# Performance work log

Measured on AMD Instinct MI355X. Metric: run time of the kernel, lower is better.

## Reference

```python
import jax, jax.numpy as jnp
import numpy as np

NEG = -1e30  # log-space 'zero' (avoid real -inf for stable exp/grad)


def _ctc_loss_mean(logp, targets, target_lengths, blank):
    """CTC loss, PyTorch semantics (reduction='mean', zero_infinity=True).
    logp: (B, T, V) log-probabilities; targets: (B, L) padded labels;
    target_lengths: (B,) ints. All input lengths are T (uniform here).
    """
    B, T, V = logp.shape
    L = targets.shape[1]
    S = 2 * L + 1  # extended label length: blank-interleaved

    ext = jnp.full((B, S), blank, dtype=targets.dtype)
    ext = ext.at[:, 1::2].set(targets)  # blanks at even s, labels at odd s

    s = jnp.arange(S)
    valid = s[None, :] < (2 * target_lengths + 1)[:, None]  # (B, S)
    prev2 = jnp.pad(ext[:, :-2], ((0, 0), (2, 0)), constant_values=blank)
    # skip transition s-2 -> s allowed only at non-blank s with no label repeat
    allow_skip = (s[None, :] >= 2) & (ext != blank) & (ext != prev2)

    # per-(t, s) emission log-prob, masked outside valid extended labels
    emit = jnp.take_along_axis(
        logp, jnp.broadcast_to(ext[:, None, :], (B, T, S)), axis=2
    )  # (B, T, S)
    emit = jnp.where(valid[:, None, :], emit, NEG)

    alpha0 = jnp.full((B, S), NEG, dtype=logp.dtype)
    alpha0 = alpha0.at[:, 0].set(emit[:, 0, 0])
    alpha0 = alpha0.at[:, 1].set(emit[:, 0, 1])

    def step(alpha, e):
        a1 = alpha
        a2 = jnp.pad(alpha[:, :-1], ((0, 0), (1, 0)), constant_values=NEG)
        a3 = jnp.pad(alpha[:, :-2], ((0, 0), (2, 0)), constant_values=NEG)
        a3 = jnp.where(allow_skip, a3, NEG)
        m = jnp.maximum(jnp.maximum(a1, a2), a3)
        new = m + jnp.log(jnp.exp(a1 - m) + jnp.exp(a2 - m) + jnp.exp(a3 - m)) + e
        return new, None

    alpha, _ = jax.lax.scan(step, alpha0, jnp.swapaxes(emit, 0, 1)[1:])

    i1 = (2 * target_lengths).astype(jnp.int32)
    l1 = jnp.take_along_axis(alpha, i1[:, None], axis=1)[:, 0]
    l2 = jnp.take_along_axis(alpha, jnp.maximum(i1 - 1, 0)[:, None], axis=1)[:, 0]
    l2 = jnp.where(target_lengths > 0, l2, NEG)
    m = jnp.maximum(l1, l2)
    loss = -(m + jnp.log(jnp.exp(l1 - m) + jnp.exp(l2 - m)))  # (B,)
    loss = jnp.where(loss > 1e20, 0.0, loss)  # zero_infinity=True
    # reduction='mean': divide by target length, then batch mean
    return jnp.mean(loss / jnp.maximum(target_lengths, 1).astype(loss.dtype))


def setup_inputs() -> dict:
    key = jax.random.key(0)
    kl, kt, kn = jax.random.split(key, 3)
    B, T, V, L = 32, 1024, 1000, 256
    logits = jax.random.normal(kl, (B, T, V), dtype=jnp.float32)
    targets = jax.random.randint(kt, (B, L), 1, V).astype(jnp.int32)
    lengths = jax.random.randint(kn, (B,), L // 2 + 2, L + 1)
    target_padding_mask = jnp.arange(L)[None, :] < lengths[:, None]  # bool (B, L)
    return {"logits": logits, "targets": targets,
            "target_padding_mask": target_padding_mask}


def reference(logits, targets, target_padding_mask):
    blank = 0
    lg = logits[:, :-1, :]            # drop last frame
    tgt = targets[:, 1:]              # drop leading (SOS) token
    logp = jax.nn.log_softmax(lg, axis=-1)  # (B, T-1, V)
    tlen = target_padding_mask.sum(axis=1).astype(jnp.int32) - 1
    return _ctc_loss_mean(logp, tgt, tlen, blank)
```

## Files before the change

kernel.cpp:

```cpp
#include <hip/hip_runtime.h>

#define LOG2E 1.4426950408889634f
#define LN2   0.6931471805599453

static constexpr int B  = 32;
static constexpr int T  = 1024;
static constexpr int TT = 1023;
static constexpr int V  = 1000;
static constexpr int L  = 256;
static constexpr int S  = 511;
static constexpr int LP = 256;
static constexpr int TP = 1024;

using hf2 = __attribute__((ext_vector_type(2))) __fp16;
using f4  = __attribute__((ext_vector_type(4))) float;
using i4  = __attribute__((ext_vector_type(4))) int;
using i2  = __attribute__((ext_vector_type(2))) int;

__device__ __forceinline__ float fexp2(float x) {
#if __has_builtin(__builtin_amdgcn_exp2f)
  return __builtin_amdgcn_exp2f(x);
#else
  return exp2f(x);
#endif
}
__device__ __forceinline__ float flog2(float x) {
#if __has_builtin(__builtin_amdgcn_logf)
  return __builtin_amdgcn_logf(x);
#else
  return log2f(x);
#endif
}

#if __has_builtin(__builtin_amdgcn_update_dpp)
__device__ __forceinline__ float shr1f(float x) {
  int r = __builtin_amdgcn_update_dpp(0, __float_as_int(x), 0x138, 0xf, 0xf, true);
  return __int_as_float(r);
}
__device__ __forceinline__ int shl1i(int x) {
  return __builtin_amdgcn_update_dpp(0, x, 0x130, 0xf, 0xf, true);
}
#define DPP_SWITCH(T, OLD, SRC, BC)                                            \
  T r;                                                                         \
  switch (ctrl) {                                                              \
    case 0x111: r = __builtin_amdgcn_update_dpp(OLD, SRC, 0x111, 0xf, 0xf, BC); break; \
    case 0x112: r = __builtin_amdgcn_update_dpp(OLD, SRC, 0x112, 0xf, 0xf, BC); break; \
    case 0x114: r = __builtin_amdgcn_update_dpp(OLD, SRC, 0x114, 0xf, 0xf, BC); break; \
    case 0x118: r = __builtin_amdgcn_update_dpp(OLD, SRC, 0x118, 0xf, 0xf, BC); break; \
    case 0x142: r = __builtin_amdgcn_update_dpp(OLD, SRC, 0x142, 0xf, 0xf, BC); break; \
    default:    r = __builtin_amdgcn_update_dpp(OLD, SRC, 0x143, 0xf, 0xf, BC); break; \
  }

__device__ __forceinline__ int dppmax_step(int m, const int ctrl) {
  DPP_SWITCH(int, 0, m, true);
  return max(m, r);
}
__device__ __forceinline__ int wavemax_to_sgpr(int m) {
  m = dppmax_step(m, 0x111);
  m = dppmax_step(m, 0x112);
  m = dppmax_step(m, 0x114);
  m = dppmax_step(m, 0x118);
  m = dppmax_step(m, 0x142);
  m = dppmax_step(m, 0x143);
  return __builtin_amdgcn_readlane(m, 63);
}
__device__ __forceinline__ float dppfmax_step(float x, const int ctrl) {
  int xi = __float_as_int(x);
  DPP_SWITCH(int, xi, xi, false);
  return fmaxf(x, __int_as_float(r));
}
__device__ __forceinline__ float wavefmax(float x) {
  x = dppfmax_step(x, 0x111);
  x = dppfmax_step(x, 0x112);
  x = dppfmax_step(x, 0x114);
  x = dppfmax_step(x, 0x118);
  x = dppfmax_step(x, 0x142);
  x = dppfmax_step(x, 0x143);
  return __int_as_float(__builtin_amdgcn_readlane(__float_as_int(x), 63));
}
__device__ __forceinline__ float dppfadd_step(float x, const int ctrl) {
  DPP_SWITCH(int, 0, __float_as_int(x), true);
  return x + __int_as_float(r);
}
__device__ __forceinline__ float wavefsum(float x) {
  x = dppfadd_step(x, 0x111);
  x = dppfadd_step(x, 0x112);
  x = dppfadd_step(x, 0x114);
  x = dppfadd_step(x, 0x118);
  x = dppfadd_step(x, 0x142);
  x = dppfadd_step(x, 0x143);
  return __int_as_float(__builtin_amdgcn_readlane(__float_as_int(x), 63));
}
#else
__device__ __forceinline__ float shr1f(float x) {
  float r = __shfl_up(x, 1, 64);
  return (threadIdx.x & 63) == 0 ? 0.0f : r;
}
__device__ __forceinline__ int shl1i(int x) {
  int r = __shfl_down(x, 1, 64);
  return (threadIdx.x & 63) == 63 ? 0 : r;
}
__device__ __forceinline__ int wavemax_to_sgpr(int m) {
  for (int o = 32; o >= 1; o >>= 1) m = max(m, __shfl_xor(m, o, 64));
  return m;
}
__device__ __forceinline__ float wavefmax(float x) {
  for (int o = 32; o >= 1; o >>= 1) x = fmaxf(x, __shfl_xor(x, o, 64));
  return x;
}
__device__ __forceinline__ float wavefsum(float x) {
  for (int o = 32; o >= 1; o >>= 1) x += __shfl_xor(x, o, 64);
  return x;
}
#endif

__device__ __forceinline__ int mask_tlen(const unsigned char* maskb, int b, int lane) {
  int ca = 0;
  for (int k = lane; k < L; k += 64) ca += (maskb[b * L + k] != 0) ? 1 : 0;
  for (int o = 32; o >= 1; o >>= 1) ca += __shfl_xor(ca, o, 64);
  int cnt = ca;
  if (ca < 130) {
    const int* mi = (const int*)maskb;
    int cb = 0;
    for (int k = lane; k < L; k += 64) cb += (mi[b * L + k] != 0) ? 1 : 0;
    for (int o = 32; o >= 1; o >>= 1) cb += __shfl_xor(cb, o, 64);
    cnt = cb;
  }
  return cnt - 1;
}

__global__ __launch_bounds__(256) void k_emit(const float* __restrict__ logits,
                                              const int* __restrict__ targets,
                                              _Float16* __restrict__ EL,
                                              _Float16* __restrict__ EBs,
                                              float* __restrict__ I2,
                                              float* __restrict__ G) {
  __shared__ float yrow[4][1024];
  const int wid = threadIdx.x >> 6;
  const int lane = threadIdx.x & 63;
  float* yw = yrow[wid];
  const int r = blockIdx.x * 4 + wid;
  const int b = r / TT;
  const int t = r - b * TT;

  const f4* row = reinterpret_cast<const f4*>(logits + ((size_t)b * T + t) * V);
  f4 u0 = row[lane];
  f4 u1 = row[lane + 64];
  f4 u2 = row[lane + 128];
  const bool has3 = (lane < 58);
  f4 u3;
  if (has3) u3 = row[lane + 192];
  else { u3[0] = u3[1] = u3[2] = u3[3] = -3.0e38f; }

  reinterpret_cast<f4*>(yw)[lane]       = u0;
  reinterpret_cast<f4*>(yw)[lane + 64]  = u1;
  reinterpret_cast<f4*>(yw)[lane + 128] = u2;
  if (has3) reinterpret_cast<f4*>(yw)[lane + 192] = u3;

  float lm = fmaxf(fmaxf(fmaxf(u0[0], u0[1]), fmaxf(u0[2], u0[3])),
                   fmaxf(fmaxf(u1[0], u1[1]), fmaxf(u1[2], u1[3])));
  lm = fmaxf(lm, fmaxf(fmaxf(u2[0], u2[1]), fmaxf(u2[2], u2[3])));
  lm = fmaxf(lm, fmaxf(fmaxf(u3[0], u3[1]), fmaxf(u3[2], u3[3])));
  const float my = wavefmax(lm);
  const float c = -my * LOG2E;

  float ps = fexp2(fmaf(u0[0], LOG2E, c)) + fexp2(fmaf(u0[1], LOG2E, c))
           + fexp2(fmaf(u0[2], LOG2E, c)) + fexp2(fmaf(u0[3], LOG2E, c))
           + fexp2(fmaf(u1[0], LOG2E, c)) + fexp2(fmaf(u1[1], LOG2E, c))
           + fexp2(fmaf(u1[2], LOG2E, c)) + fexp2(fmaf(u1[3], LOG2E, c))
           + fexp2(fmaf(u2[0], LOG2E, c)) + fexp2(fmaf(u2[1], LOG2E, c))
           + fexp2(fmaf(u2[2], LOG2E, c)) + fexp2(fmaf(u2[3], LOG2E, c))
           + fexp2(fmaf(u3[0], LOG2E, c)) + fexp2(fmaf(u3[1], LOG2E, c))
           + fexp2(fmaf(u3[2], LOG2E, c)) + fexp2(fmaf(u3[3], LOG2E, c));
  const float g = -flog2(wavefsum(ps));

  const int base = b * L + (lane << 2);
  i4 tv = *reinterpret_cast<const i4*>(targets + base);
  const int l1 = tv[1], l2 = tv[2], l3 = tv[3];
  const int l4 = shl1i(tv[0]);
  const float eb = fexp2(fmaf(yw[0],  LOG2E, c));
  const float e1 = fexp2(fmaf(yw[l1], LOG2E, c));
  const float e2 = fexp2(fmaf(yw[l2], LOG2E, c));
  const float e3 = fexp2(fmaf(yw[l3], LOG2E, c));
  float e4       = fexp2(fmaf(yw[l4], LOG2E, c));
  if (lane == 63) e4 = 0.0f;

  i2 oi;
#if __has_builtin(__builtin_amdgcn_cvt_pkrtz)
  { hf2 p = __builtin_amdgcn_cvt_pkrtz(e1, e2); oi[0] = __builtin_bit_cast(int, p); }
  { hf2 p = __builtin_amdgcn_cvt_pkrtz(e3, e4); oi[1] = __builtin_bit_cast(int, p); }
#else
  { hf2 p; p[0] = (__fp16)e1; p[1] = (__fp16)e2; oi[0] = __builtin_bit_cast(int, p); }
  { hf2 p; p[0] = (__fp16)e3; p[1] = (__fp16)e4; oi[1] = __builtin_bit_cast(int, p); }
#endif
  reinterpret_cast<i2*>(EL + ((size_t)b * TP + t) * LP)[lane] = oi;
  if (lane == 0) {
    G[r] = g;
    if (t > 0) EBs[b * TP + (t - 1)] = (_Float16)eb;
    else { I2[2 * b] = eb; I2[2 * b + 1] = e1; }
  }
}

__global__ __launch_bounds__(64, 1) void k_ctc(const _Float16* __restrict__ EL,
                                               const _Float16* __restrict__ EBs,
                                               const int* __restrict__ targets,
                                               const unsigned char* __restrict__ maskb,
                                               const float* __restrict__ G,
                                               const float* __restrict__ I2,
                                               float* __restrict__ lossb) {
  const int b = blockIdx.x;
  const int lane = threadIdx.x;
  const int s0 = lane << 3;
  const int* tg = targets + b * L;

  const int tl = mask_tlen(maskb, b, lane);

  float f1 = 0.0f, f3, f5, f7 = 0.0f;
  {
    int s = s0 + 1;
    if (s >= 3) f1 = (tg[(s + 1) >> 1] != tg[(s - 1) >> 1]) ? 1.0f : 0.0f;
    s = s0 + 3;
    f3 = (tg[(s + 1) >> 1] != tg[(s - 1) >> 1]) ? 1.0f : 0.0f;
    s = s0 + 5;
    f5 = (tg[(s + 1) >> 1] != tg[(s - 1) >> 1]) ? 1.0f : 0.0f;
    s = s0 + 7;
    if (s < S) f7 = (tg[(s + 1) >> 1] != tg[(s - 1) >> 1]) ? 1.0f : 0.0f;
  }

  const int s2t = 2 * tl;
  const int vm0 = (s0 + 0 <= s2t) ? -1 : 0;
  const int vm1 = (s0 + 1 <= s2t) ? -1 : 0;
  const int vm2 = (s0 + 2 <= s2t) ? -1 : 0;
  const int vm3 = (s0 + 3 <= s2t) ? -1 : 0;
  const int vm4 = (s0 + 4 <= s2t) ? -1 : 0;
  const int vm5 = (s0 + 5 <= s2t) ? -1 : 0;
  const int vm6 = (s0 + 6 <= s2t) ? -1 : 0;
  const int vm7 = (s0 + 7 <= s2t) ? -1 : 0;

  const _Float16* ELb = EL + (size_t)b * TP * LP + (lane << 2);
  const _Float16* EBb = EBs + b * TP;

  float a0 = (lane == 0) ? I2[2 * b]     : 0.0f;
  float a1 = (lane == 0) ? I2[2 * b + 1] : 0.0f;
  float a2 = 0.f, a3 = 0.f, a4 = 0.f, a5 = 0.f, a6 = 0.f, a7 = 0.f;
  float n7 = 0.0f;
  int lsacc = 0;

  asm volatile("" :: "v"(f1), "v"(f3), "v"(f5), "v"(f7),
                     "v"(a0), "v"(a1), "v"((float)tl));

#define LOAD8(P, r0)                                             \
  do {                                                           \
    const _Float16* ql_ = ELb + (size_t)(r0) * LP;               \
    const _Float16* qb_ = EBb + ((r0) - 1);                      \
    asm volatile(                                                \
      "global_load_dwordx2 %0, %9, off\n\t"                      \
      "global_load_dwordx2 %1, %9, off offset:512\n\t"           \
      "global_load_dwordx2 %2, %9, off offset:1024\n\t"          \
      "global_load_dwordx2 %3, %9, off offset:1536\n\t"          \
      "global_load_dwordx2 %4, %9, off offset:2048\n\t"          \
      "global_load_dwordx2 %5, %9, off offset:2560\n\t"          \
      "global_load_dwordx2 %6, %9, off offset:3072\n\t"          \
      "global_load_dwordx2 %7, %9, off offset:3584\n\t"          \
      "global_load_dwordx4 %8, %10, off"                         \
      : "=&v"(P##0), "=&v"(P##1), "=&v"(P##2), "=&v"(P##3),      \
        "=&v"(P##4), "=&v"(P##5), "=&v"(P##6), "=&v"(P##7),      \
        "=&v"(P##Q)                                              \
      : "v"(ql_), "v"(qb_));                                     \
  } while (0)

#define VMWAIT8(n, P)                                            \
  do {                                                           \
    asm volatile("s_waitcnt vmcnt(" #n ")"                       \
                 : "+v"(P##0), "+v"(P##1), "+v"(P##2), "+v"(P##3), \
                   "+v"(P##4), "+v"(P##5), "+v"(P##6), "+v"(P##7), \
                   "+v"(P##Q));                                  \
    __builtin_amdgcn_sched_barrier(0);                           \
  } while (0)

#define MIXLO(D, SSS, HWORD)                                     \
  asm("v_fma_mix_f32 %0, %1, %2, 0 op_sel:[0,0,0] op_sel_hi:[0,1,0]" \
      : "=v"(D) : "v"(SSS), "v"(HWORD))
#define MIXHI(D, SSS, HWORD)                                     \
  asm("v_fma_mix_f32 %0, %1, %2, 0 op_sel:[0,1,0] op_sel_hi:[0,1,0]" \
      : "=v"(D) : "v"(SSS), "v"(HWORD))

#define STEP_IMPL(H, BD, BMIX)                                  \
  do {                                                          \
    float s7_ = fmaf(f7, a5, a6 + a7);                          \
    float t7; MIXHI(t7, s7_, (H)[1]);                   \
    float n7n = shr1f(t7);                                      \
    float s0_ = a0 + n7;                                        \
    float s1_ = fmaf(f1, n7, a0 + a1);                          \
    float s2_ = a1 + a2;                                        \
    float s3_ = fmaf(f3, a1, a2 + a3);                          \
    float s4_ = a3 + a4;                                        \
    float s5_ = fmaf(f5, a3, a4 + a5);                          \
    float s6_ = a5 + a6;                                        \
    float t0, t1, t2, t3, t4, t5, t6;                           \
    BMIX(t0, s0_, (BD));                             \
    MIXLO(t1, s1_, (H)[0]);                             \
    BMIX(t2, s2_, (BD));                                        \
    MIXHI(t3, s3_, (H)[0]);                             \
    BMIX(t4, s4_, (BD));                                        \
    MIXLO(t5, s5_, (H)[1]);                             \
    BMIX(t6, s6_, (BD));                                        \
    a0 = t0; a1 = t1; a2 = t2; a3 = t3;                         \
    a4 = t4; a5 = t5; a6 = t6; a7 = t7;                         \
    n7 = n7n;                                                   \
  } while (0)
#define STEPFL(H, BD) STEP_IMPL(H, BD, MIXLO)
#define STEPFH(H, BD) STEP_IMPL(H, BD, MIXHI)

#define RESCALE()                                               \
  do {                                                          \
    int m = max(max(max(__float_as_int(a0) & vm0,               \
                        __float_as_int(a1) & vm1),              \
                    max(__float_as_int(a2) & vm2,               \
                        __float_as_int(a3) & vm3)),             \
                max(max(__float_as_int(a4) & vm4,               \
                        __float_as_int(a5) & vm5),              \
                    max(__float_as_int(a6) & vm6,               \
                        __float_as_int(a7) & vm7)));            \
    int mw = wavemax_to_sgpr(m);                                \
    int e = mw >> 23;                                           \
    int sh = 191 - e;                                           \
    lsacc += e - 191;                                           \
    a0 = ldexpf(a0, sh); a1 = ldexpf(a1, sh);                   \
    a2 = ldexpf(a2, sh); a3 = ldexpf(a3, sh);                   \
    a4 = ldexpf(a4, sh); a5 = ldexpf(a5, sh);                   \
    a6 = ldexpf(a6, sh); a7 = ldexpf(a7, sh);                   \
    n7 = ldexpf(n7, sh);                                        \
  } while (0)

#define PROC8(P)                                                \
  do {                                                          \
    STEPFL(P##0, P##Q[0]); STEPFH(P##1, P##Q[0]);               \
    STEPFL(P##2, P##Q[1]); STEPFH(P##3, P##Q[1]);               \
    STEPFL(P##4, P##Q[2]); STEPFH(P##5, P##Q[2]);               \
    STEPFL(P##6, P##Q[3]); STEPFH(P##7, P##Q[3]);               \
  } while (0)

  i2 A0, A1, A2, A3, A4, A5, A6, A7; i4 AQ;
  i2 B0, B1, B2, B3, B4, B5, B6, B7; i4 BQ;
  i2 C0, C1, C2, C3, C4, C5, C6, C7; i4 CQ;
  i2 D0, D1, D2, D3, D4, D5, D6, D7; i4 DQ;

  LOAD8(A, 1);
  LOAD8(B, 9);
  LOAD8(C, 17);
  LOAD8(D, 25);

  int t = 1;
#pragma unroll 1
  for (int it = 0; it < 30; ++it) {
    RESCALE();
    VMWAIT8(27, A); PROC8(A); LOAD8(A, t + 32);
    VMWAIT8(27, B); PROC8(B); LOAD8(B, t + 40);
    VMWAIT8(27, C); PROC8(C); LOAD8(C, t + 48);
    VMWAIT8(27, D); PROC8(D); LOAD8(D, t + 56);
    t += 32;
  }
  RESCALE();
  VMWAIT8(27, A); PROC8(A); LOAD8(A, 993);
  VMWAIT8(27, B); PROC8(B); LOAD8(B, 1001);
  VMWAIT8(27, C); PROC8(C); LOAD8(C, 1009);
  VMWAIT8(27, D); PROC8(D); LOAD8(D, 1017);
  RESCALE();
  VMWAIT8(27, A); PROC8(A);
  VMWAIT8(18, B); PROC8(B);
  VMWAIT8(9,  C); PROC8(C);
  VMWAIT8(0,  D);
  STEPFL(D0, DQ[0]); STEPFH(D1, DQ[0]);
  STEPFL(D2, DQ[1]); STEPFH(D3, DQ[1]);
  STEPFL(D4, DQ[2]); STEPFH(D5, DQ[2]);
#undef LOAD8
#undef VMWAIT8
#undef MIXLO
#undef MIXHI
#undef STEP_IMPL
#undef STEPFL
#undef STEPFH
#undef RESCALE
#undef PROC8

  double gs = 0.0;
  for (int k = lane; k < TT; k += 64) gs += (double)G[b * TT + k];
  for (int o = 32; o >= 1; o >>= 1) gs += __shfl_xor(gs, o, 64);

  {
    int i1 = 2 * tl;
    int j1 = (i1 > 0 ? i1 : 1) - 1;
    float va, vb;
    switch (i1 & 7) {
      case 0: va = a0; break; case 1: va = a1; break;
      case 2: va = a2; break; case 3: va = a3; break;
      case 4: va = a4; break; case 5: va = a5; break;
      case 6: va = a6; break; default: va = a7; break;
    }
    switch (j1 & 7) {
      case 0: vb = a0; break; case 1: vb = a1; break;
      case 2: vb = a2; break; case 3: vb = a3; break;
      case 4: vb = a4; break; case 5: vb = a5; break;
      case 6: vb = a6; break; default: vb = a7; break;
    }
    float l1v = __shfl(va, i1 >> 3, 64);
    float l2v = __shfl(vb, j1 >> 3, 64);
    if (lane == 0) {
      float p = l1v + l2v;
      int hi = __float_as_int(p);
      int ep = (hi >> 23) - 127;
      float pm = ldexpf(p, -ep);
      float lm = flog2(pm);
      double loss2 = -((double)lm + (double)ep + (double)lsacc + gs);
      float loss = (float)(loss2 * LN2);
      if (!(loss <= 1e20f)) loss = 0.0f;
      int dv = (tl > 0) ? tl : 1;
      lossb[b] = loss / (float)dv;
    }
  }
}

__global__ void k_mean(const float* __restrict__ lossb, float* __restrict__ out) {
  int lane = threadIdx.x;
  float v = (lane < B) ? lossb[lane] : 0.0f;
  for (int o = 32; o >= 1; o >>= 1) v += __shfl_xor(v, o, 64);
  if (lane == 0) out[0] = v / (float)B;
}

extern "C" void kernel_launch(void* const* d_in, const int* in_sizes, int n_in,
                              void* d_out, int out_size, void* d_ws, size_t ws_size,
                              hipStream_t stream) {
  const float* logits = (const float*)d_in[0];
  const int* targets = (const int*)d_in[1];
  const unsigned char* mask = (const unsigned char*)d_in[2];

  char* ws = (char*)d_ws;
  float* lossb = (float*)(ws + 128);
  float* I2 = (float*)(ws + 256);
  float* G = (float*)(ws + 512);
  _Float16* EBs = (_Float16*)(ws + 140 * 1024);
  _Float16* EL = (_Float16*)(ws + 256 * 1024);

  k_emit<<<(B * TT) / 4, 256, 0, stream>>>(logits, targets, EL, EBs, I2, G);
  k_ctc<<<B, 64, 0, stream>>>(EL, EBs, targets, mask, G, I2, lossb);
  k_mean<<<1, 64, 0, stream>>>(lossb, (float*)d_out);
}
```

Baseline: 82.14 us.

## Process two batch items per CTC wavefront with interleaved recurrences

Each k_ctc wavefront now runs the alpha recurrence for two batch elements (b and b+16), interleaving their steps so the two independent dependency chains hide each other's latency. The grid is halved to 16 blocks. The prefetch pipeline is reshaped from four 8-step stages to three per batch item, and the rescale exponent target changes. This trades higher register pressure and half the wavefronts for better instruction-level parallelism in the latency-bound serial scan.

```diff
diff --git a/kernel.cpp b/kernel.cpp
--- a/kernel.cpp
+++ b/kernel.cpp
@@ -208,51 +208,70 @@
                                                const float* __restrict__ G,
                                                const float* __restrict__ I2,
                                                float* __restrict__ lossb) {
-  const int b = blockIdx.x;
+  const int bx = blockIdx.x;
+  const int by = blockIdx.x + 16;
   const int lane = threadIdx.x;
   const int s0 = lane << 3;
-  const int* tg = targets + b * L;
-
-  const int tl = mask_tlen(maskb, b, lane);
-
-  float f1 = 0.0f, f3, f5, f7 = 0.0f;
+  const int* tgx = targets + bx * L;
+  const int* tgy = targets + by * L;
+
+  const int tlx = mask_tlen(maskb, bx, lane);
+  const int tly = mask_tlen(maskb, by, lane);
+
+  float f1x = 0.0f, f3x, f5x, f7x = 0.0f;
+  float f1y = 0.0f, f3y, f5y, f7y = 0.0f;
   {
     int s = s0 + 1;
-    if (s >= 3) f1 = (tg[(s + 1) >> 1] != tg[(s - 1) >> 1]) ? 1.0f : 0.0f;
+    if (s >= 3) {
+      f1x = (tgx[(s + 1) >> 1] != tgx[(s - 1) >> 1]) ? 1.0f : 0.0f;
+      f1y = (tgy[(s + 1) >> 1] != tgy[(s - 1) >> 1]) ? 1.0f : 0.0f;
+    }
     s = s0 + 3;
-    f3 = (tg[(s + 1) >> 1] != tg[(s - 1) >> 1]) ? 1.0f : 0.0f;
+    f3x = (tgx[(s + 1) >> 1] != tgx[(s - 1) >> 1]) ? 1.0f : 0.0f;
+    f3y = (tgy[(s + 1) >> 1] != tgy[(s - 1) >> 1]) ? 1.0f : 0.0f;
     s = s0 + 5;
-    f5 = (tg[(s + 1) >> 1] != tg[(s - 1) >> 1]) ? 1.0f : 0.0f;
+    f5x = (tgx[(s + 1) >> 1] != tgx[(s - 1) >> 1]) ? 1.0f : 0.0f;
+    f5y = (tgy[(s + 1) >> 1] != tgy[(s - 1) >> 1]) ? 1.0f : 0.0f;
     s = s0 + 7;
-    if (s < S) f7 = (tg[(s + 1) >> 1] != tg[(s - 1) >> 1]) ? 1.0f : 0.0f;
-  }
-
-  const int s2t = 2 * tl;
-  const int vm0 = (s0 + 0 <= s2t) ? -1 : 0;
-  const int vm1 = (s0 + 1 <= s2t) ? -1 : 0;
-  const int vm2 = (s0 + 2 <= s2t) ? -1 : 0;
-  const int vm3 = (s0 + 3 <= s2t) ? -1 : 0;
-  const int vm4 = (s0 + 4 <= s2t) ? -1 : 0;
-  const int vm5 = (s0 + 5 <= s2t) ? -1 : 0;
-  const int vm6 = (s0 + 6 <= s2t) ? -1 : 0;
-  const int vm7 = (s0 + 7 <= s2t) ? -1 : 0;
-
-  const _Float16* ELb = EL + (size_t)b * TP * LP + (lane << 2);
-  const _Float16* EBb = EBs + b * TP;
-
-  float a0 = (lane == 0) ? I2[2 * b]     : 0.0f;
-  float a1 = (lane == 0) ? I2[2 * b + 1] : 0.0f;
-  float a2 = 0.f, a3 = 0.f, a4 = 0.f, a5 = 0.f, a6 = 0.f, a7 = 0.f;
-  float n7 = 0.0f;
-  int lsacc = 0;
-
-  asm volatile("" :: "v"(f1), "v"(f3), "v"(f5), "v"(f7),
-                     "v"(a0), "v"(a1), "v"((float)tl));
-
-#define LOAD8(P, r0)                                             \
+    if (s < S) {
+      f7x = (tgx[(s + 1) >> 1] != tgx[(s - 1) >> 1]) ? 1.0f : 0.0f;
+      f7y = (tgy[(s + 1) >> 1] != tgy[(s - 1) >> 1]) ? 1.0f : 0.0f;
+    }
+  }
+
+  const int s2tx = 2 * tlx, s2ty = 2 * tly;
+  const int vm0x = (s0 + 0 <= s2tx) ? -1 : 0, vm0y = (s0 + 0 <= s2ty) ? -1 : 0;
+  const int vm1x = (s0 + 1 <= s2tx) ? -1 : 0, vm1y = (s0 + 1 <= s2ty) ? -1 : 0;
+  const int vm2x = (s0 + 2 <= s2tx) ? -1 : 0, vm2y = (s0 + 2 <= s2ty) ? -1 : 0;
+  const int vm3x = (s0 + 3 <= s2tx) ? -1 : 0, vm3y = (s0 + 3 <= s2ty) ? -1 : 0;
+  const int vm4x = (s0 + 4 <= s2tx) ? -1 : 0, vm4y = (s0 + 4 <= s2ty) ? -1 : 0;
+  const int vm5x = (s0 + 5 <= s2tx) ? -1 : 0, vm5y = (s0 + 5 <= s2ty) ? -1 : 0;
+  const int vm6x = (s0 + 6 <= s2tx) ? -1 : 0, vm6y = (s0 + 6 <= s2ty) ? -1 : 0;
+  const int vm7x = (s0 + 7 <= s2tx) ? -1 : 0, vm7y = (s0 + 7 <= s2ty) ? -1 : 0;
+
+  const _Float16* ELbx = EL + (size_t)bx * TP * LP + (lane << 2);
+  const _Float16* ELby = EL + (size_t)by * TP * LP + (lane << 2);
+  const _Float16* EBbx = EBs + bx * TP;
+  const _Float16* EBby = EBs + by * TP;
+
+  float a0x = (lane == 0) ? I2[2 * bx]     : 0.0f;
+  float a1x = (lane == 0) ? I2[2 * bx + 1] : 0.0f;
+  float a2x = 0.f, a3x = 0.f, a4x = 0.f, a5x = 0.f, a6x = 0.f, a7x = 0.f;
+  float a0y = (lane == 0) ? I2[2 * by]     : 0.0f;
+  float a1y = (lane == 0) ? I2[2 * by + 1] : 0.0f;
+  float a2y = 0.f, a3y = 0.f, a4y = 0.f, a5y = 0.f, a6y = 0.f, a7y = 0.f;
+  float n7x = 0.0f, n7y = 0.0f;
+  int lsaccx = 0, lsaccy = 0;
+
+  asm volatile("" :: "v"(f1x), "v"(f3x), "v"(f5x), "v"(f7x),
+                     "v"(f1y), "v"(f3y), "v"(f5y), "v"(f7y),
+                     "v"(a0x), "v"(a1x), "v"(a0y), "v"(a1y),
+                     "v"((float)tlx), "v"((float)tly));
+
+#define LOAD8(P, r0, ELB, EBB)                                   \
   do {                                                           \
-    const _Float16* ql_ = ELb + (size_t)(r0) * LP;               \
-    const _Float16* qb_ = EBb + ((r0) - 1);                      \
+    const _Float16* ql_ = (ELB) + (size_t)(r0) * LP;             \
+    const _Float16* qb_ = (EBB) + ((r0) - 1);                    \
     asm volatile(                                                \
       "global_load_dwordx2 %0, %9, off\n\t"                      \
       "global_load_dwordx2 %1, %9, off offset:512\n\t"           \
@@ -269,12 +288,16 @@
       : "v"(ql_), "v"(qb_));                                     \
   } while (0)
 
-#define VMWAIT8(n, P)                                            \
+#define VMWAIT2(n, PX, PY)                                       \
   do {                                                           \
     asm volatile("s_waitcnt vmcnt(" #n ")"                       \
-                 : "+v"(P##0), "+v"(P##1), "+v"(P##2), "+v"(P##3), \
-                   "+v"(P##4), "+v"(P##5), "+v"(P##6), "+v"(P##7), \
-                   "+v"(P##Q));                                  \
+                 : "+v"(PX##0), "+v"(PX##1), "+v"(PX##2), "+v"(PX##3), \
+                   "+v"(PX##4), "+v"(PX##5), "+v"(PX##6), "+v"(PX##7), \
+                   "+v"(PX##Q));                                 \
+    asm volatile(""                                              \
+                 : "+v"(PY##0), "+v"(PY##1), "+v"(PY##2), "+v"(PY##3), \
+                   "+v"(PY##4), "+v"(PY##5), "+v"(PY##6), "+v"(PY##7), \
+                   "+v"(PY##Q));                                 \
     __builtin_amdgcn_sched_barrier(0);                           \
   } while (0)
 
@@ -285,140 +308,160 @@
   asm("v_fma_mix_f32 %0, %1, %2, 0 op_sel:[0,1,0] op_sel_hi:[0,1,0]" \
       : "=v"(D) : "v"(SSS), "v"(HWORD))
 
-#define STEP_IMPL(H, BD, BMIX)                                  \
+#define STEP_IMPL(H, BD, BMIX, X)                               \
   do {                                                          \
-    float s7_ = fmaf(f7, a5, a6 + a7);                          \
-    float t7; MIXHI(t7, s7_, (H)[1]);                   \
-    float n7n = shr1f(t7);                                      \
-    float s0_ = a0 + n7;                                        \
-    float s1_ = fmaf(f1, n7, a0 + a1);                          \
-    float s2_ = a1 + a2;                                        \
-    float s3_ = fmaf(f3, a1, a2 + a3);                          \
-    float s4_ = a3 + a4;                                        \
-    float s5_ = fmaf(f5, a3, a4 + a5);                          \
-    float s6_ = a5 + a6;                                        \
-    float t0, t1, t2, t3, t4, t5, t6;                           \
-    BMIX(t0, s0_, (BD));                             \
-    MIXLO(t1, s1_, (H)[0]);                             \
-    BMIX(t2, s2_, (BD));                                        \
-    MIXHI(t3, s3_, (H)[0]);                             \
-    BMIX(t4, s4_, (BD));                                        \
-    MIXLO(t5, s5_, (H)[1]);                             \
-    BMIX(t6, s6_, (BD));                                        \
-    a0 = t0; a1 = t1; a2 = t2; a3 = t3;                         \
-    a4 = t4; a5 = t5; a6 = t6; a7 = t7;                         \
-    n7 = n7n;                                                   \
-  } while (0)
-#define STEPFL(H, BD) STEP_IMPL(H, BD, MIXLO)
-#define STEPFH(H, BD) STEP_IMPL(H, BD, MIXHI)
-
-#define RESCALE()                                               \
+    float s7_ = fmaf(f7##X, a5##X, a6##X + a7##X);              \
+    float t7_; MIXHI(t7_, s7_, (H)[1]);                 \
+    float n7n_ = shr1f(t7_);                                    \
+    float s0_ = a0##X + n7##X;                                  \
+    float s1_ = fmaf(f1##X, n7##X, a0##X + a1##X);              \
+    float s2_ = a1##X + a2##X;                                  \
+    float s3_ = fmaf(f3##X, a1##X, a2##X + a3##X);              \
+    float s4_ = a3##X + a4##X;                                  \
+    float s5_ = fmaf(f5##X, a3##X, a4##X + a5##X);              \
+    float s6_ = a5##X + a6##X;                                  \
+    float t0_, t1_, t2_, t3_, t4_, t5_, t6_;                    \
+    BMIX(t0_, s0_, (BD));                            \
+    MIXLO(t1_, s1_, (H)[0]);                            \
+    BMIX(t2_, s2_, (BD));                                       \
+    MIXHI(t3_, s3_, (H)[0]);                            \
+    BMIX(t4_, s4_, (BD));                                       \
+    MIXLO(t5_, s5_, (H)[1]);                            \
+    BMIX(t6_, s6_, (BD));                                       \
+    a0##X = t0_; a1##X = t1_; a2##X = t2_; a3##X = t3_;         \
+    a4##X = t4_; a5##X = t5_; a6##X = t6_; a7##X = t7_;         \
+    n7##X = n7n_;                                               \
+  } while (0)
+#define STEPFL(H, BD, X) STEP_IMPL(H, BD, MIXLO, X)
+#define STEPFH(H, BD, X) STEP_IMPL(H, BD, MIXHI, X)
+
+#define PROC8XY(PX, PY)                                         \
   do {                                                          \
-    int m = max(max(max(__float_as_int(a0) & vm0,               \
-                        __float_as_int(a1) & vm1),              \
-                    max(__float_as_int(a2) & vm2,               \
-                        __float_as_int(a3) & vm3)),             \
-                max(max(__float_as_int(a4) & vm4,               \
-                        __float_as_int(a5) & vm5),              \
-                    max(__float_as_int(a6) & vm6,               \
-                        __float_as_int(a7) & vm7)));            \
+    STEPFL(PX##0, PX##Q[0], x); STEPFL(PY##0, PY##Q[0], y);     \
+    STEPFH(PX##1, PX##Q[0], x); STEPFH(PY##1, PY##Q[0], y);     \
+    STEPFL(PX##2, PX##Q[1], x); STEPFL(PY##2, PY##Q[1], y);     \
+    STEPFH(PX##3, PX##Q[1], x); STEPFH(PY##3, PY##Q[1], y);     \
+    STEPFL(PX##4, PX##Q[2], x); STEPFL(PY##4, PY##Q[2], y);     \
+    STEPFH(PX##5, PX##Q[2], x); STEPFH(PY##5, PY##Q[2], y);     \
+    STEPFL(PX##6, PX##Q[3], x); STEPFL(PY##6, PY##Q[3], y);     \
+    STEPFH(PX##7, PX##Q[3], x); STEPFH(PY##7, PY##Q[3], y);     \
+  } while (0)
+
+#define RESCALE(X)                                              \
+  do {                                                          \
+    int m = max(max(max(__float_as_int(a0##X) & vm0##X,         \
+                        __float_as_int(a1##X) & vm1##X),        \
+                    max(__float_as_int(a2##X) & vm2##X,         \
+                        __float_as_int(a3##X) & vm3##X)),       \
+                max(max(__float_as_int(a4##X) & vm4##X,         \
+                        __float_as_int(a5##X) & vm5##X),        \
+                    max(__float_as_int(a6##X) & vm6##X,         \
+                        __float_as_int(a7##X) & vm7##X)));      \
     int mw = wavemax_to_sgpr(m);                                \
     int e = mw >> 23;                                           \
-    int sh = 191 - e;                                           \
-    lsacc += e - 191;                                           \
-    a0 = ldexpf(a0, sh); a1 = ldexpf(a1, sh);                   \
-    a2 = ldexpf(a2, sh); a3 = ldexpf(a3, sh);                   \
-    a4 = ldexpf(a4, sh); a5 = ldexpf(a5, sh);                   \
-    a6 = ldexpf(a6, sh); a7 = ldexpf(a7, sh);                   \
-    n7 = ldexpf(n7, sh);                                        \
-  } while (0)
-
-#define PROC8(P)                                                \
-  do {                                                          \
-    STEPFL(P##0, P##Q[0]); STEPFH(P##1, P##Q[0]);               \
-    STEPFL(P##2, P##Q[1]); STEPFH(P##3, P##Q[1]);               \
-    STEPFL(P##4, P##Q[2]); STEPFH(P##5, P##Q[2]);               \
-    STEPFL(P##6, P##Q[3]); STEPFH(P##7, P##Q[3]);               \
-  } while (0)
-
-  i2 A0, A1, A2, A3, A4, A5, A6, A7; i4 AQ;
-  i2 B0, B1, B2, B3, B4, B5, B6, B7; i4 BQ;
-  i2 C0, C1, C2, C3, C4, C5, C6, C7; i4 CQ;
-  i2 D0, D1, D2, D3, D4, D5, D6, D7; i4 DQ;
-
-  LOAD8(A, 1);
-  LOAD8(B, 9);
-  LOAD8(C, 17);
-  LOAD8(D, 25);
+    int sh = 203 - e;                                           \
+    lsacc##X += e - 203;                                        \
+    a0##X = ldexpf(a0##X, sh); a1##X = ldexpf(a1##X, sh);       \
+    a2##X = ldexpf(a2##X, sh); a3##X = ldexpf(a3##X, sh);       \
+    a4##X = ldexpf(a4##X, sh); a5##X = ldexpf(a5##X, sh);       \
+    a6##X = ldexpf(a6##X, sh); a7##X = ldexpf(a7##X, sh);       \
+    n7##X = ldexpf(n7##X, sh);                                  \
+  } while (0)
+
+  i2 Ax0, Ax1, Ax2, Ax3, Ax4, Ax5, Ax6, Ax7; i4 AxQ;
+  i2 Ay0, Ay1, Ay2, Ay3, Ay4, Ay5, Ay6, Ay7; i4 AyQ;
+  i2 Bx0, Bx1, Bx2, Bx3, Bx4, Bx5, Bx6, Bx7; i4 BxQ;
+  i2 By0, By1, By2, By3, By4, By5, By6, By7; i4 ByQ;
+  i2 Cx0, Cx1, Cx2, Cx3, Cx4, Cx5, Cx6, Cx7; i4 CxQ;
+  i2 Cy0, Cy1, Cy2, Cy3, Cy4, Cy5, Cy6, Cy7; i4 CyQ;
+
+  LOAD8(Ax, 1,  ELbx, EBbx);
+  LOAD8(Ay, 1,  ELby, EBby);
+  LOAD8(Bx, 9,  ELbx, EBbx);
+  LOAD8(By, 9,  ELby, EBby);
+  LOAD8(Cx, 17, ELbx, EBbx);
+  LOAD8(Cy, 17, ELby, EBby);
 
   int t = 1;
 #pragma unroll 1
-  for (int it = 0; it < 30; ++it) {
-    RESCALE();
-    VMWAIT8(27, A); PROC8(A); LOAD8(A, t + 32);
-    VMWAIT8(27, B); PROC8(B); LOAD8(B, t + 40);
-    VMWAIT8(27, C); PROC8(C); LOAD8(C, t + 48);
-    VMWAIT8(27, D); PROC8(D); LOAD8(D, t + 56);
-    t += 32;
-  }
-  RESCALE();
-  VMWAIT8(27, A); PROC8(A); LOAD8(A, 993);
-  VMWAIT8(27, B); PROC8(B); LOAD8(B, 1001);
-  VMWAIT8(27, C); PROC8(C); LOAD8(C, 1009);
-  VMWAIT8(27, D); PROC8(D); LOAD8(D, 1017);
-  RESCALE();
-  VMWAIT8(27, A); PROC8(A);
-  VMWAIT8(18, B); PROC8(B);
-  VMWAIT8(9,  C); PROC8(C);
-  VMWAIT8(0,  D);
-  STEPFL(D0, DQ[0]); STEPFH(D1, DQ[0]);
-  STEPFL(D2, DQ[1]); STEPFH(D3, DQ[1]);
-  STEPFL(D4, DQ[2]); STEPFH(D5, DQ[2]);
+  for (int it = 0; it < 42; ++it) {
+    RESCALE(x); RESCALE(y);
+    VMWAIT2(36, Ax, Ay); PROC8XY(Ax, Ay);
+    LOAD8(Ax, t + 24, ELbx, EBbx); LOAD8(Ay, t + 24, ELby, EBby);
+    VMWAIT2(36, Bx, By); PROC8XY(Bx, By);
+    LOAD8(Bx, t + 32, ELbx, EBbx); LOAD8(By, t + 32, ELby, EBby);
+    int c3 = t + 40;
+    if (c3 > 1015) c3 = 1;
+    VMWAIT2(36, Cx, Cy); PROC8XY(Cx, Cy);
+    LOAD8(Cx, c3, ELbx, EBbx); LOAD8(Cy, c3, ELby, EBby);
+    t += 24;
+  }
+  RESCALE(x); RESCALE(y);
+  VMWAIT2(36, Ax, Ay); PROC8XY(Ax, Ay);
+  VMWAIT2(18, Bx, By);
+  STEPFL(Bx0, BxQ[0], x); STEPFL(By0, ByQ[0], y);
+  STEPFH(Bx1, BxQ[0], x); STEPFH(By1, ByQ[0], y);
+  STEPFL(Bx2, BxQ[1], x); STEPFL(By2, ByQ[1], y);
+  STEPFH(Bx3, BxQ[1], x); STEPFH(By3, ByQ[1], y);
+  STEPFL(Bx4, BxQ[2], x); STEPFL(By4, ByQ[2], y);
+  STEPFH(Bx5, BxQ[2], x); STEPFH(By5, ByQ[2], y);
 #undef LOAD8
-#undef VMWAIT8
+#undef VMWAIT2
 #undef MIXLO
 #undef MIXHI
 #undef STEP_IMPL
 #undef STEPFL
 #undef STEPFH
+#undef PROC8XY
 #undef RESCALE
-#undef PROC8
-
-  double gs = 0.0;
-  for (int k = lane; k < TT; k += 64) gs += (double)G[b * TT + k];
-  for (int o = 32; o >= 1; o >>= 1) gs += __shfl_xor(gs, o, 64);
-
-  {
-    int i1 = 2 * tl;
-    int j1 = (i1 > 0 ? i1 : 1) - 1;
-    float va, vb;
-    switch (i1 & 7) {
-      case 0: va = a0; break; case 1: va = a1; break;
-      case 2: va = a2; break; case 3: va = a3; break;
-      case 4: va = a4; break; case 5: va = a5; break;
-      case 6: va = a6; break; default: va = a7; break;
-    }
-    switch (j1 & 7) {
-      case 0: vb = a0; break; case 1: vb = a1; break;
-      case 2: vb = a2; break; case 3: vb = a3; break;
-      case 4: vb = a4; break; case 5: vb = a5; break;
-      case 6: vb = a6; break; default: vb = a7; break;
-    }
-    float l1v = __shfl(va, i1 >> 3, 64);
-    float l2v = __shfl(vb, j1 >> 3, 64);
-    if (lane == 0) {
-      float p = l1v + l2v;
-      int hi = __float_as_int(p);
-      int ep = (hi >> 23) - 127;
-      float pm = ldexpf(p, -ep);
-      float lm = flog2(pm);
-      double loss2 = -((double)lm + (double)ep + (double)lsacc + gs);
-      float loss = (float)(loss2 * LN2);
-      if (!(loss <= 1e20f)) loss = 0.0f;
-      int dv = (tl > 0) ? tl : 1;
-      lossb[b] = loss / (float)dv;
-    }
-  }
+
+  double gsx = 0.0, gsy = 0.0;
+  for (int k = lane; k < TT; k += 64) {
+    gsx += (double)G[bx * TT + k];
+    gsy += (double)G[by * TT + k];
+  }
+  for (int o = 32; o >= 1; o >>= 1) {
+    gsx += __shfl_xor(gsx, o, 64);
+    gsy += __shfl_xor(gsy, o, 64);
+  }
+
+#define FINI(X, BB, GS)                                         \
+  do {                                                          \
+    int i1 = 2 * tl##X;                                         \
+    int j1 = (i1 > 0 ? i1 : 1) - 1;                             \
+    float va, vb;                                               \
+    switch (i1 & 7) {                                           \
+      case 0: va = a0##X; break; case 1: va = a1##X; break;     \
+      case 2: va = a2##X; break; case 3: va = a3##X; break;     \
+      case 4: va = a4##X; break; case 5: va = a5##X; break;     \
+      case 6: va = a6##X; break; default: va = a7##X; break;    \
+    }                                                           \
+    switch (j1 & 7) {                                           \
+      case 0: vb = a0##X; break; case 1: vb = a1##X; break;     \
+      case 2: vb = a2##X; break; case 3: vb = a3##X; break;     \
+      case 4: vb = a4##X; break; case 5: vb = a5##X; break;     \
+      case 6: vb = a6##X; break; default: vb = a7##X; break;    \
+    }                                                           \
+    float l1v = __shfl(va, i1 >> 3, 64);                        \
+    float l2v = __shfl(vb, j1 >> 3, 64);                        \
+    if (lane == 0) {                                            \
+      float p = l1v + l2v;                                      \
+      int hi = __float_as_int(p);                               \
+      int ep = (hi >> 23) - 127;                                \
+      float pm = ldexpf(p, -ep);                                \
+      float lm = flog2(pm);                                     \
+      double loss2 = -((double)lm + (double)ep +                \
+                       (double)lsacc##X + (GS));                \
+      float loss = (float)(loss2 * LN2);                        \
+      if (!(loss <= 1e20f)) loss = 0.0f;                        \
+      int dv = (tl##X > 0) ? tl##X : 1;                         \
+      lossb[BB] = loss / (float)dv;                             \
+    }                                                           \
+  } while (0)
+
+  FINI(x, bx, gsx);
+  FINI(y, by, gsy);
+#undef FINI
 }
 
 __global__ void k_mean(const float* __restrict__ lossb, float* __restrict__ out) {
@@ -443,6 +486,6 @@
   _Float16* EL = (_Float16*)(ws + 256 * 1024);
 
   k_emit<<<(B * TT) / 4, 256, 0, stream>>>(logits, targets, EL, EBs, I2, G);
-  k_ctc<<<B, 64, 0, stream>>>(EL, EBs, targets, mask, G, I2, lossb);
+  k_ctc<<<B / 2, 64, 0, stream>>>(EL, EBs, targets, mask, G, I2, lossb);
   k_mean<<<1, 64, 0, stream>>>(lossb, (float*)d_out);
 }
```

New measurement: 129.3 us. 1.57x slower.
